# Optimization experiments

Measured on AMD Instinct MI355X. Metric: run time of the kernel, lower is better.

The kernel has to match this reference:

```python
import jax, jax.numpy as jnp
import numpy as np

B, CH, T, D = 16, 64, 2048, 1  # d must be 1 (tf.squeeze(x, axis=-1))
F = 8  # conv filters


def setup_inputs() -> dict:
    key = jax.random.key(0)
    k1, k2, k3, k4 = jax.random.split(key, 4)
    return {
        "x": jax.random.normal(k1, (B, CH, T, D), dtype=jnp.float32),
        "w1": jax.random.normal(k2, (D, F), dtype=jnp.float32) * 0.1,
        "b1": jnp.zeros((F,), dtype=jnp.float32),
        "w2": jax.random.normal(k3, (D, F), dtype=jnp.float32) * 0.1,
        "b2": jnp.zeros((F,), dtype=jnp.float32),
        "gamma": jax.random.normal(k4, (1,), dtype=jnp.float32) * 0.1,
    }


def reference(x, w1, b1, w2, b2, gamma):
    b, ch, t, d = x.shape
    # 1x1 Conv2D == per-position matmul over channel dim; then Permute((2,1,3)) + Reshape((t,-1))
    q = (jnp.matmul(x, w1) + b1)  # (b, ch, t, F)
    k = (jnp.matmul(x, w2) + b2)  # (b, ch, t, F)
    q = jnp.transpose(q, (0, 2, 1, 3)).reshape(b, t, ch * q.shape[-1])  # (b, t, ch*F)
    k = jnp.transpose(k, (0, 2, 1, 3)).reshape(b, t, ch * k.shape[-1])  # (b, t, ch*F)
    energy = jnp.einsum('btf,bsf->bts', q, k)  # (b, t, t)
    max_h = jnp.max(energy, axis=2, keepdims=True)
    min_h = jnp.min(energy, axis=2, keepdims=True)
    energy = (energy - min_h) / (max_h - min_h + 1e-8)
    attention = jax.nn.softmax(energy, axis=-1)  # (b, t, t)
    x_sq = x[..., 0]  # (b, ch, t)
    # matmul(x_sq, attention, transpose_b=True): out[b,c,i] = sum_j x_sq[b,c,j] * attention[b,i,j]
    mixed = jnp.einsum('bcj,bij->bci', x_sq, attention)  # (b, ch, t)
    return gamma[0] * mixed[..., None] + x  # (b, ch, t, 1)
```

## Files before the change

### kernel.cpp

```cpp
#include <hip/hip_runtime.h>
#include <hip/hip_bf16.h>

#define NB 16
#define NCH 64
#define NT 2048
#define SPLIT 4
#define JQ (NT / SPLIT)
#define NTILE (JQ / 64)
#define PSTR 72

typedef __attribute__((ext_vector_type(8))) short bf8;
typedef __attribute__((ext_vector_type(4))) short bf4;
typedef __attribute__((ext_vector_type(4))) float f4;

#if defined(__has_builtin)
#if __has_builtin(__builtin_amdgcn_exp2f)
#define EXP2(x) __builtin_amdgcn_exp2f(x)
#else
#define EXP2(x) __expf((x) * 0.69314718056f)
#endif
#else
#define EXP2(x) __expf((x) * 0.69314718056f)
#endif

static __device__ __forceinline__ short f2b(float f) {
    unsigned u = __float_as_uint(f);
    u += 0x7fffu + ((u >> 16) & 1u);
    return (short)(u >> 16);
}
static __device__ __forceinline__ float b2f(short s) {
    return __uint_as_float(((unsigned)(unsigned short)s) << 16);
}

__global__ __launch_bounds__(256)
void prep_k(const float* __restrict__ x, float* __restrict__ Xs,
            short* __restrict__ xT, short* __restrict__ xn) {
    __shared__ float T[NCH][65];
    const int b = blockIdx.y, t0 = blockIdx.x * 64;
    const int tid = threadIdx.x;
    const float* xb = x + (size_t)b * NCH * NT;

    const int tt = (tid & 15) * 4;
    #pragma unroll
    for (int co = 0; co < 4; ++co) {
        int c = co * 16 + (tid >> 4);
        float4 v = *reinterpret_cast<const float4*>(&xb[(size_t)c * NT + t0 + tt]);
        T[c][tt] = v.x; T[c][tt + 1] = v.y; T[c][tt + 2] = v.z; T[c][tt + 3] = v.w;
        bf4 w; w[0] = f2b(v.x); w[1] = f2b(v.y); w[2] = f2b(v.z); w[3] = f2b(v.w);
        *reinterpret_cast<bf4*>(&xn[((size_t)b * NCH + c) * NT + t0 + tt]) = w;
    }
    __syncthreads();
    if (tid < 64) {
        float s = 0.f;
        #pragma unroll
        for (int c = 0; c < NCH; ++c) s += T[c][tid];
        Xs[b * NT + t0 + tid] = s;
    }
    const int row = tid >> 2, cs = (tid & 3) * 16;
    bf8 v0, v1;
    #pragma unroll
    for (int u = 0; u < 8; ++u) v0[u] = f2b(T[cs + u][row]);
    #pragma unroll
    for (int u = 0; u < 8; ++u) v1[u] = f2b(T[cs + 8 + u][row]);
    short* dst = xT + ((size_t)b * NT + t0 + row) * NCH + cs;
    *reinterpret_cast<bf8*>(dst) = v0;
    *reinterpret_cast<bf8*>(dst + 8) = v1;
}

__global__ __launch_bounds__(256)
void attn6_k(const float* __restrict__ w1, const float* __restrict__ b1p,
             const float* __restrict__ w2, const float* __restrict__ gp,
             const float* __restrict__ Xs, const short* __restrict__ xT,
             const short* __restrict__ xn, const float* __restrict__ x,
             float* __restrict__ out) {
    __shared__ short pool[4 * 32 * PSTR];
    __shared__ float mergeMn[4][2][16];
    __shared__ float mergeMx[4][2][16];
    __shared__ float mergePS[4][2][16];

    const int b  = blockIdx.y;
    const int i0 = blockIdx.x * 32;
    const int tid  = threadIdx.x;
    const int h    = tid >> 6;
    const int lane = tid & 63;
    const int lq = lane >> 4, ln = lane & 15;

    short* Pw = pool + h * 32 * PSTR;
    short* mergeAcc = pool;

    float s11 = 0.f, s2b1 = 0.f;
    #pragma unroll
    for (int f = 0; f < 8; ++f) {
        s11  += w1[f] * w2[f];
        s2b1 += b1p[f] * w2[f];
    }
    const float g = gp[0];

    const short* xTb = xT + (size_t)b * NT * NCH;
    const short* xnb = xn + (size_t)b * NCH * NT;
    const float* xb  = x + (size_t)b * NCH * NT;

    bf8 Bg[2][2];
    #pragma unroll
    for (int s = 0; s < 2; ++s)
        #pragma unroll
        for (int kk = 0; kk < 2; ++kk)
            Bg[s][kk] = *reinterpret_cast<const bf8*>(
                xTb + (size_t)(i0 + s * 16 + ln) * NCH + kk * 32 + lq * 8);

    float rmin[2] = {3.0e38f, 3.0e38f}, rmax[2] = {-3.0e38f, -3.0e38f};

    for (int t = 0; t < NTILE; ++t) {
        const int j0t = h * JQ + t * 64;
        const short* abase = xTb + (size_t)j0t * NCH;
        #pragma unroll
        for (int jn = 0; jn < 4; ++jn) {
            float4 xv = *reinterpret_cast<const float4*>(Xs + b * NT + j0t + jn * 16 + lq * 4);
            float t1[4] = { s2b1 * xv.x, s2b1 * xv.y, s2b1 * xv.z, s2b1 * xv.w };
            const short* ap = abase + (size_t)(jn * 16 + ln) * NCH + lq * 8;
            bf8 a0 = *reinterpret_cast<const bf8*>(ap);
            bf8 a1 = *reinterpret_cast<const bf8*>(ap + 32);
            #pragma unroll
            for (int s = 0; s < 2; ++s) {
                f4 acc = {0.f, 0.f, 0.f, 0.f};
                acc = __builtin_amdgcn_mfma_f32_16x16x32_bf16(a0, Bg[s][0], acc, 0, 0, 0);
                acc = __builtin_amdgcn_mfma_f32_16x16x32_bf16(a1, Bg[s][1], acc, 0, 0, 0);
                float e0 = fmaf(s11, acc[0], t1[0]);
                float e1 = fmaf(s11, acc[1], t1[1]);
                float e2 = fmaf(s11, acc[2], t1[2]);
                float e3 = fmaf(s11, acc[3], t1[3]);
                rmin[s] = fminf(rmin[s], fminf(fminf(e0, e1), fminf(e2, e3)));
                rmax[s] = fmaxf(rmax[s], fmaxf(fmaxf(e0, e1), fmaxf(e2, e3)));
            }
        }
    }

    #pragma unroll
    for (int s = 0; s < 2; ++s) {
        rmin[s] = fminf(rmin[s], __shfl_xor(rmin[s], 16, 64));
        rmin[s] = fminf(rmin[s], __shfl_xor(rmin[s], 32, 64));
        rmax[s] = fmaxf(rmax[s], __shfl_xor(rmax[s], 16, 64));
        rmax[s] = fmaxf(rmax[s], __shfl_xor(rmax[s], 32, 64));
    }
    if (lane < 16) {
        #pragma unroll
        for (int s = 0; s < 2; ++s) {
            mergeMn[h][s][ln] = rmin[s];
            mergeMx[h][s][ln] = rmax[s];
        }
    }
    __syncthreads();

    float A[2], KI[2], inv2s[2];
    #pragma unroll
    for (int s = 0; s < 2; ++s) {
        float a = mergeMn[0][s][ln], bb = mergeMx[0][s][ln];
        #pragma unroll
        for (int w = 1; w < 4; ++w) {
            a  = fminf(a, mergeMn[w][s][ln]);
            bb = fmaxf(bb, mergeMx[w][s][ln]);
        }
        const float inv = 1.f / (bb - a + 1e-8f);
        inv2s[s] = inv * 1.44269504f;
        A[s]  = s11 * inv2s[s];
        KI[s] = -a * inv2s[s];
    }

    f4 macc[4][2];
    #pragma unroll
    for (int cb = 0; cb < 4; ++cb)
        #pragma unroll
        for (int s = 0; s < 2; ++s)
            macc[cb][s] = (f4){0.f, 0.f, 0.f, 0.f};
    float ps[2] = {0.f, 0.f};

    for (int t = 0; t < NTILE; ++t) {
        const int j0t = h * JQ + t * 64;
        const short* abase = xTb + (size_t)j0t * NCH;
        #pragma unroll
        for (int jn = 0; jn < 4; ++jn) {
            float4 xv = *reinterpret_cast<const float4*>(Xs + b * NT + j0t + jn * 16 + lq * 4);
            float t1[4] = { s2b1 * xv.x, s2b1 * xv.y, s2b1 * xv.z, s2b1 * xv.w };
            const short* ap = abase + (size_t)(jn * 16 + ln) * NCH + lq * 8;
            bf8 a0 = *reinterpret_cast<const bf8*>(ap);
            bf8 a1 = *reinterpret_cast<const bf8*>(ap + 32);
            #pragma unroll
            for (int s = 0; s < 2; ++s) {
                f4 acc = {0.f, 0.f, 0.f, 0.f};
                acc = __builtin_amdgcn_mfma_f32_16x16x32_bf16(a0, Bg[s][0], acc, 0, 0, 0);
                acc = __builtin_amdgcn_mfma_f32_16x16x32_bf16(a1, Bg[s][1], acc, 0, 0, 0);
                float D0 = fmaf(t1[0], inv2s[s], KI[s]);
                float D1 = fmaf(t1[1], inv2s[s], KI[s]);
                float D2 = fmaf(t1[2], inv2s[s], KI[s]);
                float D3 = fmaf(t1[3], inv2s[s], KI[s]);
                float p0 = EXP2(fmaf(A[s], acc[0], D0));
                float p1 = EXP2(fmaf(A[s], acc[1], D1));
                float p2 = EXP2(fmaf(A[s], acc[2], D2));
                float p3 = EXP2(fmaf(A[s], acc[3], D3));
                ps[s] += (p0 + p1) + (p2 + p3);
                __hip_bfloat162 q0 = __float22bfloat162_rn(make_float2(p0, p1));
                __hip_bfloat162 q1 = __float22bfloat162_rn(make_float2(p2, p3));
                uint2 uu = make_uint2(*reinterpret_cast<unsigned*>(&q0),
                                      *reinterpret_cast<unsigned*>(&q1));
                *reinterpret_cast<uint2*>(&Pw[(s * 16 + ln) * PSTR + jn * 16 + lq * 4]) = uu;
            }
        }
        bf8 Pf[2][2];
        #pragma unroll
        for (int s = 0; s < 2; ++s)
            #pragma unroll
            for (int kk = 0; kk < 2; ++kk)
                Pf[s][kk] = *reinterpret_cast<const bf8*>(
                    &Pw[(s * 16 + ln) * PSTR + kk * 32 + lq * 8]);
        #pragma unroll
        for (int cb = 0; cb < 4; ++cb) {
            const short* mp = xnb + (size_t)(cb * 16 + ln) * NT + j0t + lq * 8;
            bf8 m0 = *reinterpret_cast<const bf8*>(mp);
            bf8 m1 = *reinterpret_cast<const bf8*>(mp + 32);
            #pragma unroll
            for (int s = 0; s < 2; ++s) {
                macc[cb][s] = __builtin_amdgcn_mfma_f32_16x16x32_bf16(m0, Pf[s][0], macc[cb][s], 0, 0, 0);
                macc[cb][s] = __builtin_amdgcn_mfma_f32_16x16x32_bf16(m1, Pf[s][1], macc[cb][s], 0, 0, 0);
            }
        }
    }

    #pragma unroll
    for (int s = 0; s < 2; ++s) {
        ps[s] += __shfl_xor(ps[s], 16, 64);
        ps[s] += __shfl_xor(ps[s], 32, 64);
    }
    if (lane < 16) {
        #pragma unroll
        for (int s = 0; s < 2; ++s) mergePS[h][s][ln] = ps[s];
    }
    __syncthreads();

    #pragma unroll
    for (int cb = 0; cb < 4; ++cb)
        #pragma unroll
        for (int s = 0; s < 2; ++s) {
            __hip_bfloat162 q0 = __float22bfloat162_rn(make_float2(macc[cb][s][0], macc[cb][s][1]));
            __hip_bfloat162 q1 = __float22bfloat162_rn(make_float2(macc[cb][s][2], macc[cb][s][3]));
            uint2 uu = make_uint2(*reinterpret_cast<unsigned*>(&q0),
                                  *reinterpret_cast<unsigned*>(&q1));
            *reinterpret_cast<uint2*>(
                &mergeAcc[(h * 32 + s * 16 + ln) * 64 + cb * 16 + lq * 4]) = uu;
        }
    __syncthreads();

    float rowSum[2];
    #pragma unroll
    for (int s = 0; s < 2; ++s) {
        float v = 0.f;
        #pragma unroll
        for (int w = 0; w < 4; ++w) v += mergePS[w][s][ln];
        rowSum[s] = v;
    }

    #pragma unroll
    for (int s = 0; s < 2; ++s) {
        const int i = i0 + s * 16 + ln;
        float tot[4] = {0.f, 0.f, 0.f, 0.f};
        #pragma unroll
        for (int w = 0; w < 4; ++w) {
            bf4 v = *reinterpret_cast<const bf4*>(
                &mergeAcc[(w * 32 + s * 16 + ln) * 64 + h * 16 + lq * 4]);
            tot[0] += b2f(v[0]); tot[1] += b2f(v[1]);
            tot[2] += b2f(v[2]); tot[3] += b2f(v[3]);
        }
        const float sc = g / rowSum[s];
        #pragma unroll
        for (int r = 0; r < 4; ++r) {
            const int c = h * 16 + lq * 4 + r;
            out[((size_t)b * NCH + c) * NT + i] = fmaf(sc, tot[r], xb[(size_t)c * NT + i]);
        }
    }
}

extern "C" void kernel_launch(void* const* d_in, const int* in_sizes, int n_in,
                              void* d_out, int out_size, void* d_ws, size_t ws_size,
                              hipStream_t stream) {
    const float* x     = (const float*)d_in[0];
    const float* w1    = (const float*)d_in[1];
    const float* b1    = (const float*)d_in[2];
    const float* w2    = (const float*)d_in[3];
    const float* gamma = (const float*)d_in[5];
    float* out = (float*)d_out;

    float* Xs = (float*)d_ws;
    short* xT = (short*)((char*)d_ws + (size_t)NB * NT * 4);
    short* xn = (short*)((char*)d_ws + (size_t)NB * NT * 4
                         + (size_t)NB * NT * NCH * 2);

    hipLaunchKernelGGL(prep_k, dim3(NT / 64, NB), dim3(256), 0, stream, x, Xs, xT, xn);
    hipLaunchKernelGGL(attn6_k, dim3(NT / 32, NB), dim3(256), 0, stream,
                       w1, b1, w2, gamma, Xs, xT, xn, x, out);
}
```

Baseline: 119.3 us.

## Split fused attention into separate min/max and softmax-mix kernels

The single fused kernel, which ran a min/max pass and then an exp/mix pass per 32-row block, is split in two. A 512-thread min/max kernel writes row min/max to workspace, and a second kernel handles 16 rows per block using the precomputed stats. The intent is more blocks with fewer registers per thread, for better occupancy and parallelism. The cost is an extra launch, an extra workspace round trip, and B-fragment reloads, since each row block now recomputes QK^T across two kernels.

```diff
diff --git a/kernel.cpp b/kernel.cpp
--- a/kernel.cpp
+++ b/kernel.cpp
@@ -4,10 +4,7 @@
 #define NB 16
 #define NCH 64
 #define NT 2048
-#define SPLIT 4
-#define JQ (NT / SPLIT)
-#define NTILE (JQ / 64)
-#define PSTR 72
+#define PSTR 66
 
 typedef __attribute__((ext_vector_type(8))) short bf8;
 typedef __attribute__((ext_vector_type(4))) short bf4;
@@ -67,26 +64,20 @@
     *reinterpret_cast<bf8*>(dst + 8) = v1;
 }
 
-__global__ __launch_bounds__(256)
-void attn6_k(const float* __restrict__ w1, const float* __restrict__ b1p,
-             const float* __restrict__ w2, const float* __restrict__ gp,
-             const float* __restrict__ Xs, const short* __restrict__ xT,
-             const short* __restrict__ xn, const float* __restrict__ x,
-             float* __restrict__ out) {
-    __shared__ short pool[4 * 32 * PSTR];
-    __shared__ float mergeMn[4][2][16];
-    __shared__ float mergeMx[4][2][16];
-    __shared__ float mergePS[4][2][16];
+__global__ __launch_bounds__(512)
+void minmax_k(const float* __restrict__ w1, const float* __restrict__ b1p,
+              const float* __restrict__ w2,
+              const float* __restrict__ Xs, const short* __restrict__ xT,
+              float* __restrict__ rowMin, float* __restrict__ rowMax) {
+    __shared__ float mergeMn[8][2][16];
+    __shared__ float mergeMx[8][2][16];
 
     const int b  = blockIdx.y;
     const int i0 = blockIdx.x * 32;
     const int tid  = threadIdx.x;
-    const int h    = tid >> 6;
+    const int w    = tid >> 6;
     const int lane = tid & 63;
     const int lq = lane >> 4, ln = lane & 15;
-
-    short* Pw = pool + h * 32 * PSTR;
-    short* mergeAcc = pool;
 
     float s11 = 0.f, s2b1 = 0.f;
     #pragma unroll
@@ -94,11 +85,8 @@
         s11  += w1[f] * w2[f];
         s2b1 += b1p[f] * w2[f];
     }
-    const float g = gp[0];
 
     const short* xTb = xT + (size_t)b * NT * NCH;
-    const short* xnb = xn + (size_t)b * NCH * NT;
-    const float* xb  = x + (size_t)b * NCH * NT;
 
     bf8 Bg[2][2];
     #pragma unroll
@@ -110,8 +98,8 @@
 
     float rmin[2] = {3.0e38f, 3.0e38f}, rmax[2] = {-3.0e38f, -3.0e38f};
 
-    for (int t = 0; t < NTILE; ++t) {
-        const int j0t = h * JQ + t * 64;
+    for (int t = 0; t < 4; ++t) {
+        const int j0t = w * 256 + t * 64;
         const short* abase = xTb + (size_t)j0t * NCH;
         #pragma unroll
         for (int jn = 0; jn < 4; ++jn) {
@@ -145,136 +133,142 @@
     if (lane < 16) {
         #pragma unroll
         for (int s = 0; s < 2; ++s) {
-            mergeMn[h][s][ln] = rmin[s];
-            mergeMx[h][s][ln] = rmax[s];
-        }
-    }
-    __syncthreads();
-
-    float A[2], KI[2], inv2s[2];
-    #pragma unroll
-    for (int s = 0; s < 2; ++s) {
-        float a = mergeMn[0][s][ln], bb = mergeMx[0][s][ln];
-        #pragma unroll
-        for (int w = 1; w < 4; ++w) {
-            a  = fminf(a, mergeMn[w][s][ln]);
-            bb = fmaxf(bb, mergeMx[w][s][ln]);
-        }
-        const float inv = 1.f / (bb - a + 1e-8f);
-        inv2s[s] = inv * 1.44269504f;
-        A[s]  = s11 * inv2s[s];
-        KI[s] = -a * inv2s[s];
-    }
-
-    f4 macc[4][2];
-    #pragma unroll
-    for (int cb = 0; cb < 4; ++cb)
-        #pragma unroll
-        for (int s = 0; s < 2; ++s)
-            macc[cb][s] = (f4){0.f, 0.f, 0.f, 0.f};
-    float ps[2] = {0.f, 0.f};
-
-    for (int t = 0; t < NTILE; ++t) {
-        const int j0t = h * JQ + t * 64;
+            mergeMn[w][s][ln] = rmin[s];
+            mergeMx[w][s][ln] = rmax[s];
+        }
+    }
+    __syncthreads();
+    if (tid < 32) {
+        float a = mergeMn[0][tid >> 4][tid & 15];
+        #pragma unroll
+        for (int u = 1; u < 8; ++u) a = fminf(a, mergeMn[u][tid >> 4][tid & 15]);
+        rowMin[b * NT + i0 + tid] = a;
+    } else if (tid < 64) {
+        const int ii = tid - 32;
+        float a = mergeMx[0][ii >> 4][ii & 15];
+        #pragma unroll
+        for (int u = 1; u < 8; ++u) a = fmaxf(a, mergeMx[u][ii >> 4][ii & 15]);
+        rowMax[b * NT + i0 + ii] = a;
+    }
+}
+
+__global__ __launch_bounds__(256)
+void mixed_k(const float* __restrict__ w1, const float* __restrict__ b1p,
+             const float* __restrict__ w2, const float* __restrict__ gp,
+             const float* __restrict__ Xs, const short* __restrict__ xT,
+             const short* __restrict__ xn, const float* __restrict__ x,
+             const float* __restrict__ rowMin, const float* __restrict__ rowMax,
+             float* __restrict__ out) {
+    __shared__ short pool[4 * 16 * PSTR];
+    __shared__ float mergePS[4][16];
+
+    const int b  = blockIdx.y;
+    const int i0 = blockIdx.x * 16;
+    const int tid  = threadIdx.x;
+    const int h    = tid >> 6;
+    const int lane = tid & 63;
+    const int lq = lane >> 4, ln = lane & 15;
+
+    short* Pw = pool + h * 16 * PSTR;
+    short* mergeAcc = pool;
+
+    float s11 = 0.f, s2b1 = 0.f;
+    #pragma unroll
+    for (int f = 0; f < 8; ++f) {
+        s11  += w1[f] * w2[f];
+        s2b1 += b1p[f] * w2[f];
+    }
+    const float g = gp[0];
+
+    const short* xTb = xT + (size_t)b * NT * NCH;
+    const short* xnb = xn + (size_t)b * NCH * NT;
+    const float* xb  = x + (size_t)b * NCH * NT;
+
+    bf8 Bg[2];
+    #pragma unroll
+    for (int kk = 0; kk < 2; ++kk)
+        Bg[kk] = *reinterpret_cast<const bf8*>(
+            xTb + (size_t)(i0 + ln) * NCH + kk * 32 + lq * 8);
+
+    const float mnv = rowMin[b * NT + i0 + ln];
+    const float mxv = rowMax[b * NT + i0 + ln];
+    const float inv2 = 1.44269504f / (mxv - mnv + 1e-8f);
+    const float A  = s11 * inv2;
+    const float KI = -mnv * inv2;
+
+    f4 macc[4];
+    #pragma unroll
+    for (int cb = 0; cb < 4; ++cb) macc[cb] = (f4){0.f, 0.f, 0.f, 0.f};
+    float ps = 0.f;
+
+    for (int t = 0; t < 8; ++t) {
+        const int j0t = h * 512 + t * 64;
         const short* abase = xTb + (size_t)j0t * NCH;
         #pragma unroll
         for (int jn = 0; jn < 4; ++jn) {
             float4 xv = *reinterpret_cast<const float4*>(Xs + b * NT + j0t + jn * 16 + lq * 4);
-            float t1[4] = { s2b1 * xv.x, s2b1 * xv.y, s2b1 * xv.z, s2b1 * xv.w };
             const short* ap = abase + (size_t)(jn * 16 + ln) * NCH + lq * 8;
             bf8 a0 = *reinterpret_cast<const bf8*>(ap);
             bf8 a1 = *reinterpret_cast<const bf8*>(ap + 32);
-            #pragma unroll
-            for (int s = 0; s < 2; ++s) {
-                f4 acc = {0.f, 0.f, 0.f, 0.f};
-                acc = __builtin_amdgcn_mfma_f32_16x16x32_bf16(a0, Bg[s][0], acc, 0, 0, 0);
-                acc = __builtin_amdgcn_mfma_f32_16x16x32_bf16(a1, Bg[s][1], acc, 0, 0, 0);
-                float D0 = fmaf(t1[0], inv2s[s], KI[s]);
-                float D1 = fmaf(t1[1], inv2s[s], KI[s]);
-                float D2 = fmaf(t1[2], inv2s[s], KI[s]);
-                float D3 = fmaf(t1[3], inv2s[s], KI[s]);
-                float p0 = EXP2(fmaf(A[s], acc[0], D0));
-                float p1 = EXP2(fmaf(A[s], acc[1], D1));
-                float p2 = EXP2(fmaf(A[s], acc[2], D2));
-                float p3 = EXP2(fmaf(A[s], acc[3], D3));
-                ps[s] += (p0 + p1) + (p2 + p3);
-                __hip_bfloat162 q0 = __float22bfloat162_rn(make_float2(p0, p1));
-                __hip_bfloat162 q1 = __float22bfloat162_rn(make_float2(p2, p3));
-                uint2 uu = make_uint2(*reinterpret_cast<unsigned*>(&q0),
-                                      *reinterpret_cast<unsigned*>(&q1));
-                *reinterpret_cast<uint2*>(&Pw[(s * 16 + ln) * PSTR + jn * 16 + lq * 4]) = uu;
-            }
-        }
-        bf8 Pf[2][2];
-        #pragma unroll
-        for (int s = 0; s < 2; ++s)
-            #pragma unroll
-            for (int kk = 0; kk < 2; ++kk)
-                Pf[s][kk] = *reinterpret_cast<const bf8*>(
-                    &Pw[(s * 16 + ln) * PSTR + kk * 32 + lq * 8]);
+            f4 acc = {0.f, 0.f, 0.f, 0.f};
+            acc = __builtin_amdgcn_mfma_f32_16x16x32_bf16(a0, Bg[0], acc, 0, 0, 0);
+            acc = __builtin_amdgcn_mfma_f32_16x16x32_bf16(a1, Bg[1], acc, 0, 0, 0);
+            float D0 = fmaf(s2b1 * xv.x, inv2, KI);
+            float D1 = fmaf(s2b1 * xv.y, inv2, KI);
+            float D2 = fmaf(s2b1 * xv.z, inv2, KI);
+            float D3 = fmaf(s2b1 * xv.w, inv2, KI);
+            float p0 = EXP2(fmaf(A, acc[0], D0));
+            float p1 = EXP2(fmaf(A, acc[1], D1));
+            float p2 = EXP2(fmaf(A, acc[2], D2));
+            float p3 = EXP2(fmaf(A, acc[3], D3));
+            ps += (p0 + p1) + (p2 + p3);
+            __hip_bfloat162 q0 = __float22bfloat162_rn(make_float2(p0, p1));
+            __hip_bfloat162 q1 = __float22bfloat162_rn(make_float2(p2, p3));
+            uint2 uu = make_uint2(*reinterpret_cast<unsigned*>(&q0),
+                                  *reinterpret_cast<unsigned*>(&q1));
+            *reinterpret_cast<uint2*>(&Pw[ln * PSTR + jn * 16 + lq * 4]) = uu;
+        }
+        bf8 Pf[2];
+        #pragma unroll
+        for (int kk = 0; kk < 2; ++kk)
+            Pf[kk] = *reinterpret_cast<const bf8*>(&Pw[ln * PSTR + kk * 32 + lq * 8]);
         #pragma unroll
         for (int cb = 0; cb < 4; ++cb) {
             const short* mp = xnb + (size_t)(cb * 16 + ln) * NT + j0t + lq * 8;
             bf8 m0 = *reinterpret_cast<const bf8*>(mp);
             bf8 m1 = *reinterpret_cast<const bf8*>(mp + 32);
-            #pragma unroll
-            for (int s = 0; s < 2; ++s) {
-                macc[cb][s] = __builtin_amdgcn_mfma_f32_16x16x32_bf16(m0, Pf[s][0], macc[cb][s], 0, 0, 0);
-                macc[cb][s] = __builtin_amdgcn_mfma_f32_16x16x32_bf16(m1, Pf[s][1], macc[cb][s], 0, 0, 0);
-            }
-        }
-    }
-
-    #pragma unroll
-    for (int s = 0; s < 2; ++s) {
-        ps[s] += __shfl_xor(ps[s], 16, 64);
-        ps[s] += __shfl_xor(ps[s], 32, 64);
-    }
-    if (lane < 16) {
-        #pragma unroll
-        for (int s = 0; s < 2; ++s) mergePS[h][s][ln] = ps[s];
-    }
-    __syncthreads();
-
-    #pragma unroll
-    for (int cb = 0; cb < 4; ++cb)
-        #pragma unroll
-        for (int s = 0; s < 2; ++s) {
-            __hip_bfloat162 q0 = __float22bfloat162_rn(make_float2(macc[cb][s][0], macc[cb][s][1]));
-            __hip_bfloat162 q1 = __float22bfloat162_rn(make_float2(macc[cb][s][2], macc[cb][s][3]));
-            uint2 uu = make_uint2(*reinterpret_cast<unsigned*>(&q0),
-                                  *reinterpret_cast<unsigned*>(&q1));
-            *reinterpret_cast<uint2*>(
-                &mergeAcc[(h * 32 + s * 16 + ln) * 64 + cb * 16 + lq * 4]) = uu;
-        }
-    __syncthreads();
-
-    float rowSum[2];
-    #pragma unroll
-    for (int s = 0; s < 2; ++s) {
-        float v = 0.f;
-        #pragma unroll
-        for (int w = 0; w < 4; ++w) v += mergePS[w][s][ln];
-        rowSum[s] = v;
-    }
-
-    #pragma unroll
-    for (int s = 0; s < 2; ++s) {
-        const int i = i0 + s * 16 + ln;
-        float tot[4] = {0.f, 0.f, 0.f, 0.f};
-        #pragma unroll
-        for (int w = 0; w < 4; ++w) {
-            bf4 v = *reinterpret_cast<const bf4*>(
-                &mergeAcc[(w * 32 + s * 16 + ln) * 64 + h * 16 + lq * 4]);
-            tot[0] += b2f(v[0]); tot[1] += b2f(v[1]);
-            tot[2] += b2f(v[2]); tot[3] += b2f(v[3]);
-        }
-        const float sc = g / rowSum[s];
-        #pragma unroll
-        for (int r = 0; r < 4; ++r) {
-            const int c = h * 16 + lq * 4 + r;
-            out[((size_t)b * NCH + c) * NT + i] = fmaf(sc, tot[r], xb[(size_t)c * NT + i]);
-        }
+            macc[cb] = __builtin_amdgcn_mfma_f32_16x16x32_bf16(m0, Pf[0], macc[cb], 0, 0, 0);
+            macc[cb] = __builtin_amdgcn_mfma_f32_16x16x32_bf16(m1, Pf[1], macc[cb], 0, 0, 0);
+        }
+    }
+
+    ps += __shfl_xor(ps, 16, 64);
+    ps += __shfl_xor(ps, 32, 64);
+    if (lane < 16) mergePS[h][ln] = ps;
+    __syncthreads();
+
+    #pragma unroll
+    for (int cb = 0; cb < 4; ++cb) {
+        __hip_bfloat162 q0 = __float22bfloat162_rn(make_float2(macc[cb][0], macc[cb][1]));
+        __hip_bfloat162 q1 = __float22bfloat162_rn(make_float2(macc[cb][2], macc[cb][3]));
+        uint2 uu = make_uint2(*reinterpret_cast<unsigned*>(&q0),
+                              *reinterpret_cast<unsigned*>(&q1));
+        *reinterpret_cast<uint2*>(&mergeAcc[(h * 16 + ln) * PSTR + cb * 16 + lq * 4]) = uu;
+    }
+    __syncthreads();
+
+    float rowSum = mergePS[0][ln] + mergePS[1][ln] + mergePS[2][ln] + mergePS[3][ln];
+    const float sc = g / rowSum;
+
+    const int i = i0 + ln;
+    #pragma unroll
+    for (int r = 0; r < 4; ++r) {
+        const int c = h * 16 + lq * 4 + r;
+        float tot = 0.f;
+        #pragma unroll
+        for (int u = 0; u < 4; ++u)
+            tot += b2f(mergeAcc[(u * 16 + ln) * PSTR + c]);
+        out[((size_t)b * NCH + c) * NT + i] = fmaf(sc, tot, xb[(size_t)c * NT + i]);
     }
 }
 
@@ -288,12 +282,16 @@
     const float* gamma = (const float*)d_in[5];
     float* out = (float*)d_out;
 
-    float* Xs = (float*)d_ws;
-    short* xT = (short*)((char*)d_ws + (size_t)NB * NT * 4);
-    short* xn = (short*)((char*)d_ws + (size_t)NB * NT * 4
-                         + (size_t)NB * NT * NCH * 2);
+    char* p = (char*)d_ws;
+    float* Xs     = (float*)p;            p += (size_t)NB * NT * 4;
+    short* xT     = (short*)p;            p += (size_t)NB * NT * NCH * 2;
+    short* xn     = (short*)p;            p += (size_t)NB * NT * NCH * 2;
+    float* rowMin = (float*)p;            p += (size_t)NB * NT * 4;
+    float* rowMax = (float*)p;
 
     hipLaunchKernelGGL(prep_k, dim3(NT / 64, NB), dim3(256), 0, stream, x, Xs, xT, xn);
-    hipLaunchKernelGGL(attn6_k, dim3(NT / 32, NB), dim3(256), 0, stream,
-                       w1, b1, w2, gamma, Xs, xT, xn, x, out);
-}
+    hipLaunchKernelGGL(minmax_k, dim3(NT / 32, NB), dim3(512), 0, stream,
+                       w1, b1, w2, Xs, xT, rowMin, rowMax);
+    hipLaunchKernelGGL(mixed_k, dim3(NT / 16, NB), dim3(256), 0, stream,
+                       w1, b1, w2, gamma, Xs, xT, xn, x, rowMin, rowMax, out);
+}
```

New measurement: 172.7 us. 44.7% more time.

## Double-buffer per-wave P tiles to overlap gram/exp with mixing MFMAs

Applied to the files above, without the earlier changes.

Splits the tile loop into a gram+exp stage and a mixing-MFMA stage. Each wave now has two LDS buffers for its probability tile, so the exp for tile t+1 is issued before the mixing for tile t, which gives the scheduler more independent work to hide latency. The LDS row pitch changes from 72 to 66 shorts to alter the bank-conflict pattern, and the s2b1 scale is folded into a precomputed constant. The cost is twice the LDS for P, and the 66-short pitch leaves the 8- and 16-byte LDS accesses unaligned on odd rows.

```diff
diff --git a/kernel.cpp b/kernel.cpp
--- a/kernel.cpp
+++ b/kernel.cpp
@@ -7,7 +7,7 @@
 #define SPLIT 4
 #define JQ (NT / SPLIT)
 #define NTILE (JQ / 64)
-#define PSTR 72
+#define PSTR 66
 
 typedef __attribute__((ext_vector_type(8))) short bf8;
 typedef __attribute__((ext_vector_type(4))) short bf4;
@@ -68,12 +68,12 @@
 }
 
 __global__ __launch_bounds__(256)
-void attn6_k(const float* __restrict__ w1, const float* __restrict__ b1p,
+void attn8_k(const float* __restrict__ w1, const float* __restrict__ b1p,
              const float* __restrict__ w2, const float* __restrict__ gp,
              const float* __restrict__ Xs, const short* __restrict__ xT,
              const short* __restrict__ xn, const float* __restrict__ x,
              float* __restrict__ out) {
-    __shared__ short pool[4 * 32 * PSTR];
+    __shared__ short pool[4 * 2 * 32 * PSTR];
     __shared__ float mergeMn[4][2][16];
     __shared__ float mergeMx[4][2][16];
     __shared__ float mergePS[4][2][16];
@@ -85,7 +85,8 @@
     const int lane = tid & 63;
     const int lq = lane >> 4, ln = lane & 15;
 
-    short* Pw = pool + h * 32 * PSTR;
+    short* P0 = pool + h * (2 * 32 * PSTR);
+    short* P1 = P0 + 32 * PSTR;
     short* mergeAcc = pool;
 
     float s11 = 0.f, s2b1 = 0.f;
@@ -151,7 +152,7 @@
     }
     __syncthreads();
 
-    float A[2], KI[2], inv2s[2];
+    float A[2], KI[2], s2i[2];
     #pragma unroll
     for (int s = 0; s < 2; ++s) {
         float a = mergeMn[0][s][ln], bb = mergeMx[0][s][ln];
@@ -160,10 +161,10 @@
             a  = fminf(a, mergeMn[w][s][ln]);
             bb = fmaxf(bb, mergeMx[w][s][ln]);
         }
-        const float inv = 1.f / (bb - a + 1e-8f);
-        inv2s[s] = inv * 1.44269504f;
-        A[s]  = s11 * inv2s[s];
-        KI[s] = -a * inv2s[s];
+        const float inv2 = 1.44269504f / (bb - a + 1e-8f);
+        A[s]   = s11 * inv2;
+        KI[s]  = -a * inv2;
+        s2i[s] = s2b1 * inv2;
     }
 
     f4 macc[4][2];
@@ -174,13 +175,12 @@
             macc[cb][s] = (f4){0.f, 0.f, 0.f, 0.f};
     float ps[2] = {0.f, 0.f};
 
-    for (int t = 0; t < NTILE; ++t) {
+    auto gram_exp = [&](int t, short* Pb) {
         const int j0t = h * JQ + t * 64;
         const short* abase = xTb + (size_t)j0t * NCH;
         #pragma unroll
         for (int jn = 0; jn < 4; ++jn) {
             float4 xv = *reinterpret_cast<const float4*>(Xs + b * NT + j0t + jn * 16 + lq * 4);
-            float t1[4] = { s2b1 * xv.x, s2b1 * xv.y, s2b1 * xv.z, s2b1 * xv.w };
             const short* ap = abase + (size_t)(jn * 16 + ln) * NCH + lq * 8;
             bf8 a0 = *reinterpret_cast<const bf8*>(ap);
             bf8 a1 = *reinterpret_cast<const bf8*>(ap + 32);
@@ -189,10 +189,10 @@
                 f4 acc = {0.f, 0.f, 0.f, 0.f};
                 acc = __builtin_amdgcn_mfma_f32_16x16x32_bf16(a0, Bg[s][0], acc, 0, 0, 0);
                 acc = __builtin_amdgcn_mfma_f32_16x16x32_bf16(a1, Bg[s][1], acc, 0, 0, 0);
-                float D0 = fmaf(t1[0], inv2s[s], KI[s]);
-                float D1 = fmaf(t1[1], inv2s[s], KI[s]);
-                float D2 = fmaf(t1[2], inv2s[s], KI[s]);
-                float D3 = fmaf(t1[3], inv2s[s], KI[s]);
+                float D0 = fmaf(xv.x, s2i[s], KI[s]);
+                float D1 = fmaf(xv.y, s2i[s], KI[s]);
+                float D2 = fmaf(xv.z, s2i[s], KI[s]);
+                float D3 = fmaf(xv.w, s2i[s], KI[s]);
                 float p0 = EXP2(fmaf(A[s], acc[0], D0));
                 float p1 = EXP2(fmaf(A[s], acc[1], D1));
                 float p2 = EXP2(fmaf(A[s], acc[2], D2));
@@ -202,16 +202,19 @@
                 __hip_bfloat162 q1 = __float22bfloat162_rn(make_float2(p2, p3));
                 uint2 uu = make_uint2(*reinterpret_cast<unsigned*>(&q0),
                                       *reinterpret_cast<unsigned*>(&q1));
-                *reinterpret_cast<uint2*>(&Pw[(s * 16 + ln) * PSTR + jn * 16 + lq * 4]) = uu;
+                *reinterpret_cast<uint2*>(&Pb[(s * 16 + ln) * PSTR + jn * 16 + lq * 4]) = uu;
             }
         }
+    };
+    auto mixed_st = [&](int t, const short* Pb) {
+        const int j0t = h * JQ + t * 64;
         bf8 Pf[2][2];
         #pragma unroll
         for (int s = 0; s < 2; ++s)
             #pragma unroll
             for (int kk = 0; kk < 2; ++kk)
                 Pf[s][kk] = *reinterpret_cast<const bf8*>(
-                    &Pw[(s * 16 + ln) * PSTR + kk * 32 + lq * 8]);
+                    &Pb[(s * 16 + ln) * PSTR + kk * 32 + lq * 8]);
         #pragma unroll
         for (int cb = 0; cb < 4; ++cb) {
             const short* mp = xnb + (size_t)(cb * 16 + ln) * NT + j0t + lq * 8;
@@ -223,7 +226,19 @@
                 macc[cb][s] = __builtin_amdgcn_mfma_f32_16x16x32_bf16(m1, Pf[s][1], macc[cb][s], 0, 0, 0);
             }
         }
-    }
+    };
+
+    gram_exp(0, P0);
+    #pragma unroll
+    for (int tp = 0; tp < 3; ++tp) {
+        gram_exp(2 * tp + 1, P1);
+        mixed_st(2 * tp,     P0);
+        gram_exp(2 * tp + 2, P0);
+        mixed_st(2 * tp + 1, P1);
+    }
+    gram_exp(7, P1);
+    mixed_st(6, P0);
+    mixed_st(7, P1);
 
     #pragma unroll
     for (int s = 0; s < 2; ++s) {
@@ -245,7 +260,7 @@
             uint2 uu = make_uint2(*reinterpret_cast<unsigned*>(&q0),
                                   *reinterpret_cast<unsigned*>(&q1));
             *reinterpret_cast<uint2*>(
-                &mergeAcc[(h * 32 + s * 16 + ln) * 64 + cb * 16 + lq * 4]) = uu;
+                &mergeAcc[(h * 32 + s * 16 + ln) * PSTR + cb * 16 + lq * 4]) = uu;
         }
     __syncthreads();
 
@@ -265,7 +280,7 @@
         #pragma unroll
         for (int w = 0; w < 4; ++w) {
             bf4 v = *reinterpret_cast<const bf4*>(
-                &mergeAcc[(w * 32 + s * 16 + ln) * 64 + h * 16 + lq * 4]);
+                &mergeAcc[(w * 32 + s * 16 + ln) * PSTR + h * 16 + lq * 4]);
             tot[0] += b2f(v[0]); tot[1] += b2f(v[1]);
             tot[2] += b2f(v[2]); tot[3] += b2f(v[3]);
         }
@@ -288,12 +303,12 @@
     const float* gamma = (const float*)d_in[5];
     float* out = (float*)d_out;
 
-    float* Xs = (float*)d_ws;
-    short* xT = (short*)((char*)d_ws + (size_t)NB * NT * 4);
-    short* xn = (short*)((char*)d_ws + (size_t)NB * NT * 4
-                         + (size_t)NB * NT * NCH * 2);
+    char* p = (char*)d_ws;
+    float* Xs = (float*)p;   p += (size_t)NB * NT * 4;
+    short* xT = (short*)p;   p += (size_t)NB * NT * NCH * 2;
+    short* xn = (short*)p;
 
     hipLaunchKernelGGL(prep_k, dim3(NT / 64, NB), dim3(256), 0, stream, x, Xs, xT, xn);
-    hipLaunchKernelGGL(attn6_k, dim3(NT / 32, NB), dim3(256), 0, stream,
+    hipLaunchKernelGGL(attn8_k, dim3(NT / 32, NB), dim3(256), 0, stream,
                        w1, b1, w2, gamma, Xs, xT, xn, x, out);
 }
```

Measured after the change: 111.6 us. 6.5% less time.
